# Kernel optimization log

Measured on AMD Instinct MI355X. Metric: run time of the kernel, lower is better.

Reference implementation:

```python
import jax, jax.numpy as jnp
import numpy as np

B, L, D, H = 2, 2048, 1024, 16
HD = D // H
SCALE = HD ** (-0.5)


def setup_inputs() -> dict:
    key = jax.random.key(0)
    ks = jax.random.split(key, 12)
    mk = lambda k, shape: (0.02 * jax.random.normal(k, shape, dtype=jnp.float32))
    return {
        "x_real": jax.random.normal(ks[0], (B, L, D), dtype=jnp.float32),
        "x_imag": jax.random.normal(ks[1], (B, L, D), dtype=jnp.float32),
        "wq_r": mk(ks[2], (D, D)),
        "wq_i": mk(ks[3], (D, D)),
        "wk_r": mk(ks[4], (D, D)),
        "wk_i": mk(ks[5], (D, D)),
        "wv_r": mk(ks[6], (D, D)),
        "wv_i": mk(ks[7], (D, D)),
        "wo_r": mk(ks[8], (D, D)),
        "wo_i": mk(ks[9], (D, D)),
        "bo_r": jnp.zeros((D,), dtype=jnp.float32),
        "bo_i": jnp.zeros((D,), dtype=jnp.float32),
    }


def _clinear(xr, xi, wr, wi):
    # (a+bi)(c+di): real = a@Wr^T - b@Wi^T ; imag = a@Wi^T + b@Wr^T
    r = xr @ wr.T - xi @ wi.T
    i = xr @ wi.T + xi @ wr.T
    return r, i


def _heads(t):
    # [B,L,D] -> [B,H,L,hd]
    return t.reshape(B, L, H, HD).transpose(0, 2, 1, 3)


def reference(x_real, x_imag, wq_r, wq_i, wk_r, wk_i, wv_r, wv_i, wo_r, wo_i, bo_r, bo_i):
    Qr, Qi = _clinear(x_real, x_imag, wq_r, wq_i)
    Kr, Ki = _clinear(x_real, x_imag, wk_r, wk_i)
    Vr, Vi = _clinear(x_real, x_imag, wv_r, wv_i)
    Qr, Qi, Kr, Ki, Vr, Vi = map(_heads, (Qr, Qi, Kr, Ki, Vr, Vi))

    # real part of complex dot product: Re(Q)Re(K)^T + Im(Q)Im(K)^T
    scores = (jnp.einsum("bhqd,bhkd->bhqk", Qr, Kr)
              + jnp.einsum("bhqd,bhkd->bhqk", Qi, Ki)) * SCALE
    causal = jnp.tril(jnp.ones((L, L), dtype=bool))
    scores = jnp.where(causal, scores, -jnp.inf)
    w = jax.nn.softmax(scores, axis=-1)

    out_r = jnp.einsum("bhqk,bhkd->bhqd", w, Vr)
    out_i = jnp.einsum("bhqk,bhkd->bhqd", w, Vi)
    merge = lambda t: t.transpose(0, 2, 1, 3).reshape(B, L, D)
    out_r, out_i = merge(out_r), merge(out_i)

    yr, yi = _clinear(out_r, out_i, wo_r, wo_i)
    return yr + bo_r, yi + bo_i
```

## Files before the change

kernel.cpp:

```cpp
#include <hip/hip_runtime.h>
#include <hip/hip_bf16.h>


using f32x4  = __attribute__((ext_vector_type(4))) float;
using short8 = __attribute__((ext_vector_type(8))) short;
using bf16_t = __hip_bfloat16;

#define AS1 __attribute__((address_space(1)))
#define AS3 __attribute__((address_space(3)))

__device__ __forceinline__ void gload_lds16(const bf16_t* g, bf16_t* l) {
  __builtin_amdgcn_global_load_lds((const AS1 unsigned int*)g, (AS3 unsigned int*)l, 16, 0, 0);
}

__device__ __forceinline__ unsigned short bfbits(float f) {
  union { bf16_t h; unsigned short u; } c; c.h = __float2bfloat16(f); return c.u;
}

__global__ void pack_x_k(const float* __restrict__ xr, const float* __restrict__ xi,
                         bf16_t* __restrict__ out) {
  const int total4 = 4096 * 2048 / 4;
  for (int idx = blockIdx.x * blockDim.x + threadIdx.x; idx < total4;
       idx += gridDim.x * blockDim.x) {
    int m = idx >> 9, k = (idx & 511) * 4;
    const float* src = (k < 1024) ? (xr + (size_t)m * 1024 + k)
                                  : (xi + (size_t)m * 1024 + (k - 1024));
    float4 v = *(const float4*)src;
    unsigned int lo = (unsigned)bfbits(v.x) | ((unsigned)bfbits(v.y) << 16);
    unsigned int hi = (unsigned)bfbits(v.z) | ((unsigned)bfbits(v.w) << 16);
    *(uint2*)(out + (size_t)idx * 4) = make_uint2(lo, hi);
  }
}

__global__ void pack_wqkv_k(const float* __restrict__ wqr, const float* __restrict__ wqi,
                            const float* __restrict__ wkr, const float* __restrict__ wki,
                            const float* __restrict__ wvr, const float* __restrict__ wvi,
                            bf16_t* __restrict__ out) {
  const int total4 = 6144 * 2048 / 4;
  for (int idx = blockIdx.x * blockDim.x + threadIdx.x; idx < total4;
       idx += gridDim.x * blockDim.x) {
    int row = idx >> 9, k = (idx & 511) * 4;
    int sec = row >> 10, r1 = row & 1023;
    bool lowk = (k < 1024);
    int kk = lowk ? k : (k - 1024);
    const float* base = wqr; float sg = 1.f;
    switch (sec) {
      case 0: base = lowk ? wqr : wqi; sg = lowk ? 1.f : -1.f; break;
      case 1: base = lowk ? wqi : wqr; break;
      case 2: base = lowk ? wkr : wki; sg = lowk ? 1.f : -1.f; break;
      case 3: base = lowk ? wki : wkr; break;
      case 4: base = lowk ? wvr : wvi; sg = lowk ? 1.f : -1.f; break;
      case 5: base = lowk ? wvi : wvr; break;
    }
    float4 v = *(const float4*)(base + (size_t)r1 * 1024 + kk);
    unsigned int lo = (unsigned)bfbits(v.x * sg) | ((unsigned)bfbits(v.y * sg) << 16);
    unsigned int hi = (unsigned)bfbits(v.z * sg) | ((unsigned)bfbits(v.w * sg) << 16);
    *(uint2*)(out + (size_t)idx * 4) = make_uint2(lo, hi);
  }
}

__global__ void pack_wo_k(const float* __restrict__ wor, const float* __restrict__ woi,
                          bf16_t* __restrict__ out) {
  const int total4 = 2048 * 2048 / 4;
  for (int idx = blockIdx.x * blockDim.x + threadIdx.x; idx < total4;
       idx += gridDim.x * blockDim.x) {
    int row = idx >> 9, k = (idx & 511) * 4;
    int sec = row >> 10, r1 = row & 1023;
    bool lowk = (k < 1024);
    int kk = lowk ? k : (k - 1024);
    const float* base; float sg = 1.f;
    if (sec == 0) { base = lowk ? wor : woi; sg = lowk ? 1.f : -1.f; }
    else          { base = lowk ? woi : wor; }
    float4 v = *(const float4*)(base + (size_t)r1 * 1024 + kk);
    unsigned int lo = (unsigned)bfbits(v.x * sg) | ((unsigned)bfbits(v.y * sg) << 16);
    unsigned int hi = (unsigned)bfbits(v.z * sg) | ((unsigned)bfbits(v.w * sg) << 16);
    *(uint2*)(out + (size_t)idx * 4) = make_uint2(lo, hi);
  }
}

__device__ __forceinline__ void gemm_core(const bf16_t* __restrict__ A,
                                          const bf16_t* __restrict__ W,
                                          int m0, int n0, f32x4 (&acc)[4][4]) {
  __shared__ __align__(16) bf16_t sA[128 * 64];
  __shared__ __align__(16) bf16_t sB[128 * 64];
  const int tid = threadIdx.x;
  const int lane = tid & 63, w = tid >> 6;
  const int wr = w >> 1, wc = w & 1;
  const int quad = lane >> 4, m16 = lane & 15;
  const int srow = w * 32 + (lane >> 3);
  const int gcol = (((lane & 7) ^ (lane >> 3)) * 8);
  const int swz7 = m16 & 7;
  for (int k0 = 0; k0 < 2048; k0 += 64) {
    __syncthreads();
#pragma unroll
    for (int i = 0; i < 4; ++i) {
      gload_lds16(A + (size_t)(m0 + srow + i * 8) * 2048 + k0 + gcol,
                  sA + (size_t)(w * 32 + i * 8) * 64 + lane * 8);
      gload_lds16(W + (size_t)(n0 + srow + i * 8) * 2048 + k0 + gcol,
                  sB + (size_t)(w * 32 + i * 8) * 64 + lane * 8);
    }
    __syncthreads();
#pragma unroll
    for (int kk = 0; kk < 2; ++kk) {
      short8 af[4], bf[4];
#pragma unroll
      for (int i = 0; i < 4; ++i)
        af[i] = *(const short8*)(sA + (wr * 64 + i * 16 + m16) * 64 +
                                 ((kk * 4 + quad) ^ swz7) * 8);
#pragma unroll
      for (int j = 0; j < 4; ++j)
        bf[j] = *(const short8*)(sB + (wc * 64 + j * 16 + m16) * 64 +
                                 ((kk * 4 + quad) ^ swz7) * 8);
#pragma unroll
      for (int i = 0; i < 4; ++i)
#pragma unroll
        for (int j = 0; j < 4; ++j)
          acc[i][j] = __builtin_amdgcn_mfma_f32_16x16x32_bf16(af[i], bf[j], acc[i][j], 0, 0, 0);
    }
  }
}

__global__ __launch_bounds__(256) void gemm_qkv_k(const bf16_t* __restrict__ A,
                                                  const bf16_t* __restrict__ W,
                                                  bf16_t* __restrict__ qk,
                                                  bf16_t* __restrict__ vt) {
  f32x4 acc[4][4] = {};
  const int m0 = blockIdx.x * 128, n0 = blockIdx.y * 128;
  gemm_core(A, W, m0, n0, acc);
  const int lane = threadIdx.x & 63, w = threadIdx.x >> 6;
  const int wr = w >> 1, wc = w & 1, quad = lane >> 4, m16 = lane & 15;
#pragma unroll
  for (int i = 0; i < 4; ++i) {
    const int rowb = m0 + wr * 64 + i * 16 + quad * 4;
#pragma unroll
    for (int j = 0; j < 4; ++j) {
      const int col = n0 + wc * 64 + j * 16 + m16;
      if (col < 4096) {
        const float sc = (col < 2048) ? 0.125f : 1.f;
#pragma unroll
        for (int r = 0; r < 4; ++r)
          qk[(size_t)(rowb + r) * 4096 + col] = __float2bfloat16(acc[i][j][r] * sc);
      } else {
        const int vcol = col - 4096;
        const int ri = vcol >> 10, dfeat = vcol & 1023;
        const int b = rowb >> 11, seq = rowb & 2047;
        const size_t vrow = (size_t)(b * 2048 + (dfeat >> 6) * 128 + ri * 64 + (dfeat & 63));
        unsigned int lo = (unsigned)bfbits(acc[i][j][0]) | ((unsigned)bfbits(acc[i][j][1]) << 16);
        unsigned int hi = (unsigned)bfbits(acc[i][j][2]) | ((unsigned)bfbits(acc[i][j][3]) << 16);
        *(uint2*)(vt + vrow * 2048 + seq) = make_uint2(lo, hi);
      }
    }
  }
}

__global__ __launch_bounds__(256) void gemm_out_k(const bf16_t* __restrict__ A,
                                                  const bf16_t* __restrict__ W,
                                                  const float* __restrict__ bor,
                                                  const float* __restrict__ boi,
                                                  float* __restrict__ out) {
  f32x4 acc[4][4] = {};
  const int m0 = blockIdx.x * 128, n0 = blockIdx.y * 128;
  gemm_core(A, W, m0, n0, acc);
  const int lane = threadIdx.x & 63, w = threadIdx.x >> 6;
  const int wr = w >> 1, wc = w & 1, quad = lane >> 4, m16 = lane & 15;
#pragma unroll
  for (int i = 0; i < 4; ++i) {
    const int rowb = m0 + wr * 64 + i * 16 + quad * 4;
#pragma unroll
    for (int j = 0; j < 4; ++j) {
      const int col = n0 + wc * 64 + j * 16 + m16;
      float bias; float* op;
      if (col < 1024) { bias = bor[col]; op = out + col; }
      else            { bias = boi[col - 1024]; op = out + 4194304 + (col - 1024); }
#pragma unroll
      for (int r = 0; r < 4; ++r)
        op[(size_t)(rowb + r) * 1024] = acc[i][j][r] + bias;
    }
  }
}

__global__ __launch_bounds__(256, 2) void attn_k(const bf16_t* __restrict__ qk,
                                                 const bf16_t* __restrict__ vt,
                                                 bf16_t* __restrict__ acat) {
  __shared__ __align__(16) bf16_t sK[64 * 128];
  __shared__ __align__(16) bf16_t sV[144 * 64];
  __shared__ __align__(16) bf16_t sP[4][2][16 * 72];
  const int tid = threadIdx.x, lane = tid & 63, w = tid >> 6;
  const int quad = lane >> 4, m16 = lane & 15;
  const int x = blockIdx.x, bh = blockIdx.y, b = bh >> 4, h = bh & 15;
  const size_t qkrow0 = (size_t)b * 2048;
  const int qA = x * 64, qB = (31 - x) * 64;
  const int nT = 32 - x;
  const int swz7 = m16 & 7;

  {
    const int rr = tid >> 4, cb = (tid & 15) * 4;
    const bf16_t v = __float2bfloat16(rr == 0 ? 1.f : 0.f);
#pragma unroll
    for (int i = 0; i < 4; ++i) sV[(128 + rr) * 64 + cb + i] = v;
  }

  short8 qfA[4], qfB[4];
  {
    const bf16_t* qa = qk + (qkrow0 + qA + w * 16 + m16) * 4096;
    const bf16_t* qb = qk + (qkrow0 + qB + w * 16 + m16) * 4096;
#pragma unroll
    for (int kk = 0; kk < 4; ++kk) {
      const int col = (kk >> 1) * 1024 + h * 64 + (kk & 1) * 32 + quad * 8;
      qfA[kk] = *(const short8*)(qa + col);
      qfB[kk] = *(const short8*)(qb + col);
    }
  }
  f32x4 oA[9], oB[9];
#pragma unroll
  for (int j = 0; j < 9; ++j) { oA[j] = (f32x4){0.f,0.f,0.f,0.f}; oB[j] = (f32x4){0.f,0.f,0.f,0.f}; }

  const int qrowA = qA + w * 16 + quad * 4;
  const int qrowB = qB + w * 16 + quad * 4;

  const int kl4 = lane >> 4, kl15 = lane & 15;
  const int vl3 = lane >> 3;
  const int vg7 = ((lane & 7) ^ vl3) * 8;

  for (int t = 0; t < nT; ++t) {
    const int k0 = t * 64;
    __syncthreads();
#pragma unroll
    for (int i = 0; i < 4; ++i) {
      const int row = w * 16 + i * 4 + kl4;
      const int g = kl15 ^ (row & 7);
      const int col = 2048 + (g >> 3) * 1024 + h * 64 + (g & 7) * 8;
      gload_lds16(qk + (qkrow0 + k0 + row) * 4096 + col,
                  sK + (size_t)(w * 16 + i * 4) * 128 + lane * 8);
    }
#pragma unroll
    for (int i = 0; i < 4; ++i) {
      const int row = w * 32 + i * 8 + vl3;
      gload_lds16(vt + ((size_t)bh * 128 + row) * 2048 + k0 + vg7,
                  sV + (size_t)(w * 32 + i * 8) * 64 + lane * 8);
    }
    __syncthreads();

    const bool aAct = (t <= x);
    const bool dgA = (t == x), dgB = (t == nT - 1);

    f32x4 sAv[4], sBv[4];
    if (aAct) {
#pragma unroll
      for (int jt = 0; jt < 4; ++jt) {
        f32x4 a1 = (f32x4){0.f,0.f,0.f,0.f}, a2 = (f32x4){0.f,0.f,0.f,0.f};
#pragma unroll
        for (int kk = 0; kk < 4; ++kk) {
          short8 kf = *(const short8*)(sK + (jt * 16 + m16) * 128 +
                                       ((kk * 4 + quad) ^ swz7) * 8);
          a1 = __builtin_amdgcn_mfma_f32_16x16x32_bf16(qfA[kk], kf, a1, 0, 0, 0);
          a2 = __builtin_amdgcn_mfma_f32_16x16x32_bf16(qfB[kk], kf, a2, 0, 0, 0);
        }
        sAv[jt] = a1; sBv[jt] = a2;
      }
    } else {
#pragma unroll
      for (int jt = 0; jt < 4; ++jt) {
        f32x4 a2 = (f32x4){0.f,0.f,0.f,0.f};
#pragma unroll
        for (int kk = 0; kk < 4; ++kk) {
          short8 kf = *(const short8*)(sK + (jt * 16 + m16) * 128 +
                                       ((kk * 4 + quad) ^ swz7) * 8);
          a2 = __builtin_amdgcn_mfma_f32_16x16x32_bf16(qfB[kk], kf, a2, 0, 0, 0);
        }
        sBv[jt] = a2;
      }
    }

    if (aAct) {
      bf16_t* pw = sP[w][0];
#pragma unroll
      for (int jt = 0; jt < 4; ++jt)
#pragma unroll
        for (int r = 0; r < 4; ++r) {
          float s = sAv[jt][r];
          if (dgA && (k0 + jt * 16 + m16 > qrowA + r)) s = -1e30f;
          pw[(quad * 4 + r) * 72 + jt * 16 + m16] = __float2bfloat16(__expf(s));
        }
    }
    {
      bf16_t* pw = sP[w][1];
#pragma unroll
      for (int jt = 0; jt < 4; ++jt)
#pragma unroll
        for (int r = 0; r < 4; ++r) {
          float s = sBv[jt][r];
          if (dgB && (k0 + jt * 16 + m16 > qrowB + r)) s = -1e30f;
          pw[(quad * 4 + r) * 72 + jt * 16 + m16] = __float2bfloat16(__expf(s));
        }
    }
    asm volatile("s_waitcnt lgkmcnt(0)" ::: "memory");

    if (aAct) {
#pragma unroll
      for (int kc = 0; kc < 2; ++kc) {
        short8 pA = *(const short8*)(sP[w][0] + m16 * 72 + kc * 32 + quad * 8);
        short8 pB = *(const short8*)(sP[w][1] + m16 * 72 + kc * 32 + quad * 8);
#pragma unroll
        for (int j = 0; j < 9; ++j) {
          short8 vf = *(const short8*)(sV + (j * 16 + m16) * 64 +
                                       ((kc * 4 + quad) ^ swz7) * 8);
          oA[j] = __builtin_amdgcn_mfma_f32_16x16x32_bf16(pA, vf, oA[j], 0, 0, 0);
          oB[j] = __builtin_amdgcn_mfma_f32_16x16x32_bf16(pB, vf, oB[j], 0, 0, 0);
        }
      }
    } else {
#pragma unroll
      for (int kc = 0; kc < 2; ++kc) {
        short8 pB = *(const short8*)(sP[w][1] + m16 * 72 + kc * 32 + quad * 8);
#pragma unroll
        for (int j = 0; j < 9; ++j) {
          short8 vf = *(const short8*)(sV + (j * 16 + m16) * 64 +
                                       ((kc * 4 + quad) ^ swz7) * 8);
          oB[j] = __builtin_amdgcn_mfma_f32_16x16x32_bf16(pB, vf, oB[j], 0, 0, 0);
        }
      }
    }
  }

#pragma unroll
  for (int part = 0; part < 2; ++part) {
    f32x4* o = part ? oB : oA;
    const int qrow = part ? qrowB : qrowA;
    float inv[4];
#pragma unroll
    for (int r = 0; r < 4; ++r)
      inv[r] = 1.f / __shfl(o[8][r], lane & 48);
#pragma unroll
    for (int j = 0; j < 8; ++j) {
      const int d = j * 16 + m16;
      const int col = (d < 64) ? (h * 64 + d) : (1024 + h * 64 + (d - 64));
#pragma unroll
      for (int r = 0; r < 4; ++r)
        acat[((size_t)b * 2048 + qrow + r) * 2048 + col] = __float2bfloat16(o[j][r] * inv[r]);
    }
  }
}

extern "C" void kernel_launch(void* const* d_in, const int* in_sizes, int n_in,
                              void* d_out, int out_size, void* d_ws, size_t ws_size,
                              hipStream_t stream) {
  const float* xr  = (const float*)d_in[0];
  const float* xi  = (const float*)d_in[1];
  const float* wqr = (const float*)d_in[2];
  const float* wqi = (const float*)d_in[3];
  const float* wkr = (const float*)d_in[4];
  const float* wki = (const float*)d_in[5];
  const float* wvr = (const float*)d_in[6];
  const float* wvi = (const float*)d_in[7];
  const float* wor = (const float*)d_in[8];
  const float* woi = (const float*)d_in[9];
  const float* bor = (const float*)d_in[10];
  const float* boi = (const float*)d_in[11];
  float* out = (float*)d_out;

  char* ws = (char*)d_ws;
  bf16_t* Xcat = (bf16_t*)(ws);
  bf16_t* Wqkv = (bf16_t*)(ws + 16777216ull);
  bf16_t* QKb  = (bf16_t*)(ws + 41943040ull);
  bf16_t* Vt   = (bf16_t*)(ws + 75497472ull);
  bf16_t* Acat = (bf16_t*)(ws + 92274688ull);
  bf16_t* Wo   = (bf16_t*)(ws + 109051904ull);

  pack_x_k<<<2048, 256, 0, stream>>>(xr, xi, Xcat);
  pack_wqkv_k<<<2048, 256, 0, stream>>>(wqr, wqi, wkr, wki, wvr, wvi, Wqkv);
  pack_wo_k<<<1024, 256, 0, stream>>>(wor, woi, Wo);
  gemm_qkv_k<<<dim3(32, 48), 256, 0, stream>>>(Xcat, Wqkv, QKb, Vt);
  attn_k<<<dim3(16, 32), 256, 0, stream>>>(QKb, Vt, Acat);
  gemm_out_k<<<dim3(32, 16), 256, 0, stream>>>(Acat, Wo, bor, boi, out);
}
```

Measured before the change: 400.6 us.

## Warp-specialize GEMM core with a producer wave and triple-buffered LDS

Replaces the synchronous load-then-compute GEMM loop with a producer/consumer scheme. A fifth wave issues async global-to-LDS loads two K-steps ahead into a 3-stage ring of 32-wide K tiles, while four consumer waves run the MFMAs. The aim is to hide global load latency behind the matrix math. In exchange it doubles the number of barriers per K, adds an idle-compute wave per block, and relies on the async LDS loads having completed before the barrier without any explicit vmcnt wait.

```diff
diff --git a/kernel.cpp b/kernel.cpp
--- a/kernel.cpp
+++ b/kernel.cpp
@@ -78,39 +78,50 @@
   }
 }
 
-__device__ __forceinline__ void gemm_core(const bf16_t* __restrict__ A,
-                                          const bf16_t* __restrict__ W,
-                                          int m0, int n0, f32x4 (&acc)[4][4]) {
-  __shared__ __align__(16) bf16_t sA[128 * 64];
-  __shared__ __align__(16) bf16_t sB[128 * 64];
-  const int tid = threadIdx.x;
-  const int lane = tid & 63, w = tid >> 6;
-  const int wr = w >> 1, wc = w & 1;
-  const int quad = lane >> 4, m16 = lane & 15;
-  const int srow = w * 32 + (lane >> 3);
-  const int gcol = (((lane & 7) ^ (lane >> 3)) * 8);
-  const int swz7 = m16 & 7;
-  for (int k0 = 0; k0 < 2048; k0 += 64) {
-    __syncthreads();
-#pragma unroll
-    for (int i = 0; i < 4; ++i) {
-      gload_lds16(A + (size_t)(m0 + srow + i * 8) * 2048 + k0 + gcol,
-                  sA + (size_t)(w * 32 + i * 8) * 64 + lane * 8);
-      gload_lds16(W + (size_t)(n0 + srow + i * 8) * 2048 + k0 + gcol,
-                  sB + (size_t)(w * 32 + i * 8) * 64 + lane * 8);
-    }
-    __syncthreads();
-#pragma unroll
-    for (int kk = 0; kk < 2; ++kk) {
+__device__ __forceinline__ void gemm_core_pc(const bf16_t* __restrict__ A,
+                                             const bf16_t* __restrict__ W,
+                                             int m0, int n0, f32x4 (&acc)[4][4]) {
+  __shared__ __align__(16) bf16_t sA[3][128 * 32];
+  __shared__ __align__(16) bf16_t sB[3][128 * 32];
+  const int tid = threadIdx.x, lane = tid & 63, w = tid >> 6;
+  constexpr int T = 2048 / 32;
+
+  if (w == 4) {
+    const int r16 = lane >> 2;
+    const int g8  = ((lane & 3) ^ (r16 & 3)) * 8;
+    const bf16_t* Ab = A + (size_t)(m0 + r16) * 2048 + g8;
+    const bf16_t* Wb = W + (size_t)(n0 + r16) * 2048 + g8;
+#define ISSUE(t, s)                                                              \
+    {                                                                            \
+      const int k0_ = (t) * 32;                                                  \
+      _Pragma("unroll")                                                          \
+      for (int i = 0; i < 8; ++i) {                                              \
+        gload_lds16(Ab + (size_t)(i * 16) * 2048 + k0_, sA[s] + i * 512 + lane * 8); \
+        gload_lds16(Wb + (size_t)(i * 16) * 2048 + k0_, sB[s] + i * 512 + lane * 8); \
+      }                                                                          \
+    }
+    ISSUE(0, 0);
+    ISSUE(1, 1);
+    for (int t = 0; t < T; ++t) {
+      __syncthreads();
+      if (t + 2 < T) ISSUE(t + 2, (t + 2) % 3);
+    }
+#undef ISSUE
+  } else {
+    const int wr = w >> 1, wc = w & 1;
+    const int quad = lane >> 4, m16 = lane & 15;
+    const int csw = (quad ^ (m16 & 3)) * 8;
+    for (int t = 0; t < T; ++t) {
+      __syncthreads();
+      const bf16_t* bA = sA[t % 3];
+      const bf16_t* bB = sB[t % 3];
       short8 af[4], bf[4];
 #pragma unroll
       for (int i = 0; i < 4; ++i)
-        af[i] = *(const short8*)(sA + (wr * 64 + i * 16 + m16) * 64 +
-                                 ((kk * 4 + quad) ^ swz7) * 8);
+        af[i] = *(const short8*)(bA + (wr * 64 + i * 16 + m16) * 32 + csw);
 #pragma unroll
       for (int j = 0; j < 4; ++j)
-        bf[j] = *(const short8*)(sB + (wc * 64 + j * 16 + m16) * 64 +
-                                 ((kk * 4 + quad) ^ swz7) * 8);
+        bf[j] = *(const short8*)(bB + (wc * 64 + j * 16 + m16) * 32 + csw);
 #pragma unroll
       for (int i = 0; i < 4; ++i)
 #pragma unroll
@@ -120,13 +131,14 @@
   }
 }
 
-__global__ __launch_bounds__(256) void gemm_qkv_k(const bf16_t* __restrict__ A,
+__global__ __launch_bounds__(320) void gemm_qkv_k(const bf16_t* __restrict__ A,
                                                   const bf16_t* __restrict__ W,
                                                   bf16_t* __restrict__ qk,
                                                   bf16_t* __restrict__ vt) {
   f32x4 acc[4][4] = {};
   const int m0 = blockIdx.x * 128, n0 = blockIdx.y * 128;
-  gemm_core(A, W, m0, n0, acc);
+  gemm_core_pc(A, W, m0, n0, acc);
+  if (threadIdx.x >= 256) return;
   const int lane = threadIdx.x & 63, w = threadIdx.x >> 6;
   const int wr = w >> 1, wc = w & 1, quad = lane >> 4, m16 = lane & 15;
 #pragma unroll
@@ -153,14 +165,15 @@
   }
 }
 
-__global__ __launch_bounds__(256) void gemm_out_k(const bf16_t* __restrict__ A,
+__global__ __launch_bounds__(320) void gemm_out_k(const bf16_t* __restrict__ A,
                                                   const bf16_t* __restrict__ W,
                                                   const float* __restrict__ bor,
                                                   const float* __restrict__ boi,
                                                   float* __restrict__ out) {
   f32x4 acc[4][4] = {};
   const int m0 = blockIdx.x * 128, n0 = blockIdx.y * 128;
-  gemm_core(A, W, m0, n0, acc);
+  gemm_core_pc(A, W, m0, n0, acc);
+  if (threadIdx.x >= 256) return;
   const int lane = threadIdx.x & 63, w = threadIdx.x >> 6;
   const int wr = w >> 1, wc = w & 1, quad = lane >> 4, m16 = lane & 15;
 #pragma unroll
@@ -370,7 +383,7 @@
   pack_x_k<<<2048, 256, 0, stream>>>(xr, xi, Xcat);
   pack_wqkv_k<<<2048, 256, 0, stream>>>(wqr, wqi, wkr, wki, wvr, wvi, Wqkv);
   pack_wo_k<<<1024, 256, 0, stream>>>(wor, woi, Wo);
-  gemm_qkv_k<<<dim3(32, 48), 256, 0, stream>>>(Xcat, Wqkv, QKb, Vt);
+  gemm_qkv_k<<<dim3(32, 48), 320, 0, stream>>>(Xcat, Wqkv, QKb, Vt);
   attn_k<<<dim3(16, 32), 256, 0, stream>>>(QKb, Vt, Acat);
-  gemm_out_k<<<dim3(32, 16), 256, 0, stream>>>(Acat, Wo, bor, boi, out);
-}
+  gemm_out_k<<<dim3(32, 16), 320, 0, stream>>>(Acat, Wo, bor, boi, out);
+}
```

After: 436.7 us. 1.09x slower.

## Drop LDS staging of K/V in attention; load fragments directly from global

Applied to the files above, without the earlier changes.

The attention kernel stops staging K and V tiles through shared memory with block-wide barriers. Each wave now reads its K and V MFMA fragments straight from global memory (relying on L2/L1 reuse), and each wave owns its own 16-row query pair, so no __syncthreads are needed. The softmax now uses exp2 with log2(e) folded into the Q scale, the row-sum column comes from an in-register ones fragment, and occupancy is raised to 3 blocks per SIMD. This trades LDS traffic and barrier stalls for redundant global/cache loads across the four waves, plus more register pressure under the tighter launch bound.

```diff
diff --git a/kernel.cpp b/kernel.cpp
--- a/kernel.cpp
+++ b/kernel.cpp
@@ -136,7 +136,7 @@
     for (int j = 0; j < 4; ++j) {
       const int col = n0 + wc * 64 + j * 16 + m16;
       if (col < 4096) {
-        const float sc = (col < 2048) ? 0.125f : 1.f;
+        const float sc = (col < 2048) ? 0.18033688f : 1.f;
 #pragma unroll
         for (int r = 0; r < 4; ++r)
           qk[(size_t)(rowb + r) * 4096 + col] = __float2bfloat16(acc[i][j][r] * sc);
@@ -179,31 +179,22 @@
   }
 }
 
-__global__ __launch_bounds__(256, 2) void attn_k(const bf16_t* __restrict__ qk,
+__global__ __launch_bounds__(256, 3) void attn_k(const bf16_t* __restrict__ qk,
                                                  const bf16_t* __restrict__ vt,
                                                  bf16_t* __restrict__ acat) {
-  __shared__ __align__(16) bf16_t sK[64 * 128];
-  __shared__ __align__(16) bf16_t sV[144 * 64];
   __shared__ __align__(16) bf16_t sP[4][2][16 * 72];
   const int tid = threadIdx.x, lane = tid & 63, w = tid >> 6;
   const int quad = lane >> 4, m16 = lane & 15;
-  const int x = blockIdx.x, bh = blockIdx.y, b = bh >> 4, h = bh & 15;
+  const int g = blockIdx.x, bh = blockIdx.y, b = bh >> 4, h = bh & 15;
+  const int p = g * 4 + w;
   const size_t qkrow0 = (size_t)b * 2048;
-  const int qA = x * 64, qB = (31 - x) * 64;
-  const int nT = 32 - x;
-  const int swz7 = m16 & 7;
-
-  {
-    const int rr = tid >> 4, cb = (tid & 15) * 4;
-    const bf16_t v = __float2bfloat16(rr == 0 ? 1.f : 0.f);
-#pragma unroll
-    for (int i = 0; i < 4; ++i) sV[(128 + rr) * 64 + cb + i] = v;
-  }
+  const int qA = p * 16, qB = (127 - p) * 16;
+  const int nT = 32 - g;
 
   short8 qfA[4], qfB[4];
   {
-    const bf16_t* qa = qk + (qkrow0 + qA + w * 16 + m16) * 4096;
-    const bf16_t* qb = qk + (qkrow0 + qB + w * 16 + m16) * 4096;
+    const bf16_t* qa = qk + (qkrow0 + qA + m16) * 4096;
+    const bf16_t* qb = qk + (qkrow0 + qB + m16) * 4096;
 #pragma unroll
     for (int kk = 0; kk < 4; ++kk) {
       const int col = (kk >> 1) * 1024 + h * 64 + (kk & 1) * 32 + quad * 8;
@@ -211,115 +202,76 @@
       qfB[kk] = *(const short8*)(qb + col);
     }
   }
+  short8 vones;
+  {
+    const short v = (m16 == 0) ? (short)0x3F80 : (short)0;
+#pragma unroll
+    for (int e = 0; e < 8; ++e) vones[e] = v;
+  }
   f32x4 oA[9], oB[9];
 #pragma unroll
   for (int j = 0; j < 9; ++j) { oA[j] = (f32x4){0.f,0.f,0.f,0.f}; oB[j] = (f32x4){0.f,0.f,0.f,0.f}; }
 
-  const int qrowA = qA + w * 16 + quad * 4;
-  const int qrowB = qB + w * 16 + quad * 4;
-
-  const int kl4 = lane >> 4, kl15 = lane & 15;
-  const int vl3 = lane >> 3;
-  const int vg7 = ((lane & 7) ^ vl3) * 8;
+  const int qrowA = qA + quad * 4, qrowB = qB + quad * 4;
+  const bf16_t* kb = qk + (qkrow0 + m16) * 4096 + 2048 + h * 64 + quad * 8;
+  const bf16_t* vb = vt + ((size_t)bh * 128 + m16) * 2048 + quad * 8;
+  bf16_t* pwA = &sP[w][0][0];
+  bf16_t* pwB = &sP[w][1][0];
 
   for (int t = 0; t < nT; ++t) {
     const int k0 = t * 64;
-    __syncthreads();
-#pragma unroll
-    for (int i = 0; i < 4; ++i) {
-      const int row = w * 16 + i * 4 + kl4;
-      const int g = kl15 ^ (row & 7);
-      const int col = 2048 + (g >> 3) * 1024 + h * 64 + (g & 7) * 8;
-      gload_lds16(qk + (qkrow0 + k0 + row) * 4096 + col,
-                  sK + (size_t)(w * 16 + i * 4) * 128 + lane * 8);
-    }
-#pragma unroll
-    for (int i = 0; i < 4; ++i) {
-      const int row = w * 32 + i * 8 + vl3;
-      gload_lds16(vt + ((size_t)bh * 128 + row) * 2048 + k0 + vg7,
-                  sV + (size_t)(w * 32 + i * 8) * 64 + lane * 8);
-    }
-    __syncthreads();
-
-    const bool aAct = (t <= x);
-    const bool dgA = (t == x), dgB = (t == nT - 1);
-
-    f32x4 sAv[4], sBv[4];
-    if (aAct) {
-#pragma unroll
-      for (int jt = 0; jt < 4; ++jt) {
-        f32x4 a1 = (f32x4){0.f,0.f,0.f,0.f}, a2 = (f32x4){0.f,0.f,0.f,0.f};
-#pragma unroll
-        for (int kk = 0; kk < 4; ++kk) {
-          short8 kf = *(const short8*)(sK + (jt * 16 + m16) * 128 +
-                                       ((kk * 4 + quad) ^ swz7) * 8);
-          a1 = __builtin_amdgcn_mfma_f32_16x16x32_bf16(qfA[kk], kf, a1, 0, 0, 0);
-          a2 = __builtin_amdgcn_mfma_f32_16x16x32_bf16(qfB[kk], kf, a2, 0, 0, 0);
-        }
-        sAv[jt] = a1; sBv[jt] = a2;
+    const bool withA = (t <= g);
+    const bool dgA = (t == g), dgB = (t == nT - 1);
+
+#pragma unroll
+    for (int jt = 0; jt < 4; ++jt) {
+      const bf16_t* kr = kb + (size_t)(k0 + jt * 16) * 4096;
+      short8 kf0 = *(const short8*)(kr);
+      short8 kf1 = *(const short8*)(kr + 32);
+      short8 kf2 = *(const short8*)(kr + 1024);
+      short8 kf3 = *(const short8*)(kr + 1024 + 32);
+      f32x4 aB = (f32x4){0.f,0.f,0.f,0.f};
+      aB = __builtin_amdgcn_mfma_f32_16x16x32_bf16(qfB[0], kf0, aB, 0, 0, 0);
+      aB = __builtin_amdgcn_mfma_f32_16x16x32_bf16(qfB[1], kf1, aB, 0, 0, 0);
+      aB = __builtin_amdgcn_mfma_f32_16x16x32_bf16(qfB[2], kf2, aB, 0, 0, 0);
+      aB = __builtin_amdgcn_mfma_f32_16x16x32_bf16(qfB[3], kf3, aB, 0, 0, 0);
+#pragma unroll
+      for (int r = 0; r < 4; ++r) {
+        float s = aB[r];
+        if (dgB && (k0 + jt * 16 + m16 > qrowB + r)) s = -1e30f;
+        pwB[(quad * 4 + r) * 72 + jt * 16 + m16] =
+            __float2bfloat16(__builtin_amdgcn_exp2f(s));
       }
-    } else {
-#pragma unroll
-      for (int jt = 0; jt < 4; ++jt) {
-        f32x4 a2 = (f32x4){0.f,0.f,0.f,0.f};
-#pragma unroll
-        for (int kk = 0; kk < 4; ++kk) {
-          short8 kf = *(const short8*)(sK + (jt * 16 + m16) * 128 +
-                                       ((kk * 4 + quad) ^ swz7) * 8);
-          a2 = __builtin_amdgcn_mfma_f32_16x16x32_bf16(qfB[kk], kf, a2, 0, 0, 0);
-        }
-        sBv[jt] = a2;
-      }
-    }
-
-    if (aAct) {
-      bf16_t* pw = sP[w][0];
-#pragma unroll
-      for (int jt = 0; jt < 4; ++jt)
+      if (withA) {
+        f32x4 aA = (f32x4){0.f,0.f,0.f,0.f};
+        aA = __builtin_amdgcn_mfma_f32_16x16x32_bf16(qfA[0], kf0, aA, 0, 0, 0);
+        aA = __builtin_amdgcn_mfma_f32_16x16x32_bf16(qfA[1], kf1, aA, 0, 0, 0);
+        aA = __builtin_amdgcn_mfma_f32_16x16x32_bf16(qfA[2], kf2, aA, 0, 0, 0);
+        aA = __builtin_amdgcn_mfma_f32_16x16x32_bf16(qfA[3], kf3, aA, 0, 0, 0);
 #pragma unroll
         for (int r = 0; r < 4; ++r) {
-          float s = sAv[jt][r];
+          float s = aA[r];
           if (dgA && (k0 + jt * 16 + m16 > qrowA + r)) s = -1e30f;
-          pw[(quad * 4 + r) * 72 + jt * 16 + m16] = __float2bfloat16(__expf(s));
-        }
-    }
-    {
-      bf16_t* pw = sP[w][1];
-#pragma unroll
-      for (int jt = 0; jt < 4; ++jt)
-#pragma unroll
-        for (int r = 0; r < 4; ++r) {
-          float s = sBv[jt][r];
-          if (dgB && (k0 + jt * 16 + m16 > qrowB + r)) s = -1e30f;
-          pw[(quad * 4 + r) * 72 + jt * 16 + m16] = __float2bfloat16(__expf(s));
-        }
-    }
-    asm volatile("s_waitcnt lgkmcnt(0)" ::: "memory");
-
-    if (aAct) {
-#pragma unroll
-      for (int kc = 0; kc < 2; ++kc) {
-        short8 pA = *(const short8*)(sP[w][0] + m16 * 72 + kc * 32 + quad * 8);
-        short8 pB = *(const short8*)(sP[w][1] + m16 * 72 + kc * 32 + quad * 8);
-#pragma unroll
-        for (int j = 0; j < 9; ++j) {
-          short8 vf = *(const short8*)(sV + (j * 16 + m16) * 64 +
-                                       ((kc * 4 + quad) ^ swz7) * 8);
-          oA[j] = __builtin_amdgcn_mfma_f32_16x16x32_bf16(pA, vf, oA[j], 0, 0, 0);
-          oB[j] = __builtin_amdgcn_mfma_f32_16x16x32_bf16(pB, vf, oB[j], 0, 0, 0);
+          pwA[(quad * 4 + r) * 72 + jt * 16 + m16] =
+              __float2bfloat16(__builtin_amdgcn_exp2f(s));
         }
       }
-    } else {
-#pragma unroll
-      for (int kc = 0; kc < 2; ++kc) {
-        short8 pB = *(const short8*)(sP[w][1] + m16 * 72 + kc * 32 + quad * 8);
-#pragma unroll
-        for (int j = 0; j < 9; ++j) {
-          short8 vf = *(const short8*)(sV + (j * 16 + m16) * 64 +
-                                       ((kc * 4 + quad) ^ swz7) * 8);
-          oB[j] = __builtin_amdgcn_mfma_f32_16x16x32_bf16(pB, vf, oB[j], 0, 0, 0);
-        }
+    }
+    asm volatile("s_waitcnt lgkmcnt(0)" ::: "memory");
+
+#pragma unroll
+    for (int kc = 0; kc < 2; ++kc) {
+      short8 pB = *(const short8*)(pwB + m16 * 72 + kc * 32 + quad * 8);
+      short8 pA;
+      if (withA) pA = *(const short8*)(pwA + m16 * 72 + kc * 32 + quad * 8);
+#pragma unroll
+      for (int j = 0; j < 8; ++j) {
+        short8 vf = *(const short8*)(vb + (size_t)(j * 16) * 2048 + k0 + kc * 32);
+        oB[j] = __builtin_amdgcn_mfma_f32_16x16x32_bf16(pB, vf, oB[j], 0, 0, 0);
+        if (withA) oA[j] = __builtin_amdgcn_mfma_f32_16x16x32_bf16(pA, vf, oA[j], 0, 0, 0);
       }
+      oB[8] = __builtin_amdgcn_mfma_f32_16x16x32_bf16(pB, vones, oB[8], 0, 0, 0);
+      if (withA) oA[8] = __builtin_amdgcn_mfma_f32_16x16x32_bf16(pA, vones, oA[8], 0, 0, 0);
     }
   }
 
```

After: 547.9 us. 36.8% more time.
